# Optimization experiments

Measured on AMD Instinct MI355X. Metric: run time of the kernel, lower is better.

The kernel has to match this reference:

```python
import jax, jax.numpy as jnp
import numpy as np

D_MODEL = 1024
N_HEADS = 16
N_KV_HEADS = 4
HEAD_DIM = D_MODEL // N_HEADS  # 64
N_REP = N_HEADS // N_KV_HEADS  # 4
THETA = 10000.0
LOGIT_CAP = 30.0
EPS = 1e-6
SCALE = HEAD_DIM ** -0.5


def rmsnorm(x, w):
    return x * jax.lax.rsqrt(jnp.mean(x * x, axis=-1, keepdims=True) + EPS) * w


def rope_tables(seq_len, dtype):
    inv_freq = 1.0 / (THETA ** (jnp.arange(0, HEAD_DIM, 2, dtype=jnp.float32) / HEAD_DIM))
    t = jnp.arange(seq_len, dtype=jnp.float32)
    freqs = jnp.outer(t, inv_freq)                      # [S, hd/2]
    emb = jnp.concatenate([freqs, freqs], axis=-1)      # [S, hd]
    return jnp.cos(emb).astype(dtype), jnp.sin(emb).astype(dtype)


def rotate_half(x):
    x1, x2 = jnp.split(x, 2, axis=-1)
    return jnp.concatenate([-x2, x1], axis=-1)


def apply_rope(x, cos, sin):
    # x: [B, H, S, hd]; cos/sin: [S, hd] broadcast over (B, H)
    return x * cos + rotate_half(x) * sin


def setup_inputs() -> dict:
    key = jax.random.key(0)
    ks = jax.random.split(key, 7)
    B, S = 4, 2048
    w = 0.02
    return {
        "x": jax.random.normal(ks[0], (B, S, D_MODEL), dtype=jnp.float32),
        "Wq": jax.random.normal(ks[1], (N_HEADS * HEAD_DIM, D_MODEL), dtype=jnp.float32) * w,
        "Wk": jax.random.normal(ks[2], (N_KV_HEADS * HEAD_DIM, D_MODEL), dtype=jnp.float32) * w,
        "Wv": jax.random.normal(ks[3], (N_KV_HEADS * HEAD_DIM, D_MODEL), dtype=jnp.float32) * w,
        "Wo": jax.random.normal(ks[4], (D_MODEL, N_HEADS * HEAD_DIM), dtype=jnp.float32) * w,
        "q_norm_w": jnp.ones((HEAD_DIM,), dtype=jnp.float32),
        "k_norm_w": jnp.ones((HEAD_DIM,), dtype=jnp.float32),
    }


def reference(x, Wq, Wk, Wv, Wo, q_norm_w, k_norm_w):
    B, S, _ = x.shape
    # projections (nn.Linear: y = x @ W^T)
    q = (x @ Wq.T).reshape(B, S, N_HEADS, HEAD_DIM).transpose(0, 2, 1, 3)      # [B,H,S,d]
    k = (x @ Wk.T).reshape(B, S, N_KV_HEADS, HEAD_DIM).transpose(0, 2, 1, 3)   # [B,Hkv,S,d]
    v = (x @ Wv.T).reshape(B, S, N_KV_HEADS, HEAD_DIM).transpose(0, 2, 1, 3)
    # QK-RMSNorm
    q = rmsnorm(q, q_norm_w)
    k = rmsnorm(k, k_norm_w)
    # RoPE
    cos, sin = rope_tables(S, x.dtype)
    q = apply_rope(q, cos, sin)
    k = apply_rope(k, cos, sin)
    # GQA expand (repeat_interleave over head dim)
    k_exp = jnp.repeat(k, N_REP, axis=1)  # [B,H,S,d]
    v_exp = jnp.repeat(v, N_REP, axis=1)
    # soft-capped attention (training path)
    scores = jnp.einsum('bhqd,bhkd->bhqk', q, k_exp) * SCALE
    scores = LOGIT_CAP * jnp.tanh(scores / LOGIT_CAP)
    causal = jnp.triu(jnp.ones((S, S), dtype=bool), k=1)  # kv_len - seq_len + 1 = 1
    scores = jnp.where(causal, -jnp.inf, scores)
    attn = jax.nn.softmax(scores, axis=-1)
    out = jnp.einsum('bhqk,bhkd->bhqd', attn, v_exp)
    out = out.transpose(0, 2, 1, 3).reshape(B, S, N_HEADS * HEAD_DIM)
    return out @ Wo.T
```

## Files before the change

### kernel.cpp

```cpp
#include <hip/hip_runtime.h>
#include <hip/hip_bf16.h>
#include <math.h>
#include <stdint.h>

#define D_MODEL 1024
#define NHEADS  16
#define NKV     4
#define HD      64
#define SEQ     2048
#define BATCH   4
#define MTOK    (BATCH*SEQ)
#define NQKV    (D_MODEL + 2*NKV*HD)
#define ASCALE  0.125f
#define CAP     30.0f

using f32x4  = __attribute__((ext_vector_type(4))) float;
using f32x2  = __attribute__((ext_vector_type(2))) float;
using bf16x8 = __attribute__((ext_vector_type(8))) short;

__device__ __forceinline__ unsigned short f2bf(float f) {
  union { float f; unsigned u; } v; v.f = f;
  unsigned u = v.u + 0x7fffu + ((v.u >> 16) & 1u);
  return (unsigned short)(u >> 16);
}
__device__ __forceinline__ unsigned short f2bf_hup(float f) {
  union { float f; unsigned u; } v; v.f = f;
  return (unsigned short)((v.u + 0x8000u) >> 16);
}
__device__ __forceinline__ float fexp2(float x) {
  return __builtin_amdgcn_exp2f(x);
}
__device__ __forceinline__ void async_copy16(void* lds, const void* g) {
  __builtin_amdgcn_global_load_lds(
      (const __attribute__((address_space(1))) unsigned int*)(uintptr_t)g,
      (__attribute__((address_space(3))) unsigned int*)(uintptr_t)lds, 16, 0, 0);
}

__global__ __launch_bounds__(256) void cvt_all(
    const float* __restrict__ x, const float* __restrict__ wq,
    const float* __restrict__ wk, const float* __restrict__ wv,
    const float* __restrict__ wo,
    unsigned short* __restrict__ xb, unsigned short* __restrict__ wqkv,
    unsigned short* __restrict__ wob) {
  const long i = (long)(blockIdx.x * 256 + threadIdx.x) * 4;
  const float* src; unsigned short* dst; long off;
  if (i < 8388608L)      { src = x;  dst = xb;             off = i; }
  else if (i < 9437184L) { src = wq; dst = wqkv;           off = i - 8388608L; }
  else if (i < 9699328L) { src = wk; dst = wqkv + 1048576; off = i - 9437184L; }
  else if (i < 9961472L) { src = wv; dst = wqkv + 1310720; off = i - 9699328L; }
  else                   { src = wo; dst = wob;            off = i - 9961472L; }
  float4 v = *(const float4*)(src + off);
  ushort4 o; o.x = f2bf(v.x); o.y = f2bf(v.y); o.z = f2bf(v.z); o.w = f2bf(v.w);
  *(ushort4*)(dst + off) = o;
}

__global__ __launch_bounds__(256) void gemm_qkv(
    const unsigned short* __restrict__ A, const unsigned short* __restrict__ B,
    const float* __restrict__ qw, const float* __restrict__ kw,
    unsigned short* __restrict__ Qn, unsigned short* __restrict__ Kn,
    unsigned short* __restrict__ Vt) {
  __shared__ __align__(16) unsigned short As[128 * 32];
  __shared__ __align__(16) unsigned short Bs[128 * 32];
  const int t = threadIdx.x;
  const int w = t >> 6, l = t & 63;
  const int mb = blockIdx.x, nb = blockIdx.y;
  const int wm = w & 1, wn = w >> 1;
  const int quad = l >> 4, ln = l & 15;
  const int K = D_MODEL;
  f32x4 acc[4][4] = {};
  const unsigned short* Ag = A + (size_t)(mb * 128 + w * 32) * K;
  const unsigned short* Bg = B + (size_t)(nb * 128 + w * 32) * K;
  char* Asw = (char*)As + w * 2048;
  char* Bsw = (char*)Bs + w * 2048;
  const int lrow = l >> 2, lcol = (l & 3) * 8;

  for (int kb = 0; kb < K; kb += 32) {
    async_copy16(Asw + l * 16,        Ag + (size_t)lrow * K + kb + lcol);
    async_copy16(Asw + 1024 + l * 16, Ag + (size_t)(16 + lrow) * K + kb + lcol);
    async_copy16(Bsw + l * 16,        Bg + (size_t)lrow * K + kb + lcol);
    async_copy16(Bsw + 1024 + l * 16, Bg + (size_t)(16 + lrow) * K + kb + lcol);
    __syncthreads();
    bf16x8 af[4], bfr[4];
#pragma unroll
    for (int mt = 0; mt < 4; ++mt)
      af[mt] = *(const bf16x8*)(As + (wm * 64 + mt * 16 + ln) * 32 + quad * 8);
#pragma unroll
    for (int nt = 0; nt < 4; ++nt)
      bfr[nt] = *(const bf16x8*)(Bs + (wn * 64 + nt * 16 + ln) * 32 + quad * 8);
#pragma unroll
    for (int mt = 0; mt < 4; ++mt)
#pragma unroll
      for (int nt = 0; nt < 4; ++nt)
        acc[mt][nt] = __builtin_amdgcn_mfma_f32_16x16x32_bf16(af[mt], bfr[nt], acc[mt][nt], 0, 0, 0);
    __syncthreads();
  }

  const int hs = nb * 2 + wn;
  const int bB = mb >> 4;
  const int sBase = ((mb & 15) * 128) + wm * 64;

  if (hs < 20) {
    const float* wgt = (hs < 16) ? qw : kw;
    float wv_[4];
#pragma unroll
    for (int nt = 0; nt < 4; ++nt) wv_[nt] = wgt[nt * 16 + ln];
    const float f0 = __expf(-(float)ln * 0.2878231366f);
    const float f1 = f0 * 0.01f;
    unsigned short* dst = (hs < 16)
        ? Qn + (size_t)(bB * 16 + hs) * SEQ * 64
        : Kn + (size_t)(bB * 4 + (hs - 16)) * SEQ * 64;
#pragma unroll
    for (int mt = 0; mt < 4; ++mt) {
#pragma unroll
      for (int r = 0; r < 4; ++r) {
        const int sTok = sBase + mt * 16 + quad * 4 + r;
        float ss = 0.f;
#pragma unroll
        for (int nt = 0; nt < 4; ++nt) ss = fmaf(acc[mt][nt][r], acc[mt][nt][r], ss);
        ss += __shfl_xor(ss, 1, 64); ss += __shfl_xor(ss, 2, 64);
        ss += __shfl_xor(ss, 4, 64); ss += __shfl_xor(ss, 8, 64);
        const float inv = rsqrtf(ss * (1.0f / 64.0f) + 1e-6f);
        float xn[4];
#pragma unroll
        for (int nt = 0; nt < 4; ++nt) xn[nt] = acc[mt][nt][r] * inv * wv_[nt];
        float sn0, cs0, sn1, cs1;
        __sincosf((float)sTok * f0, &sn0, &cs0);
        __sincosf((float)sTok * f1, &sn1, &cs1);
        const float o0 = xn[0] * cs0 - xn[2] * sn0;
        const float o1 = xn[1] * cs1 - xn[3] * sn1;
        const float o2 = xn[2] * cs0 + xn[0] * sn0;
        const float o3 = xn[3] * cs1 + xn[1] * sn1;
        const size_t ro = (size_t)sTok * 64 + ln;
        dst[ro]      = f2bf(o0);
        dst[ro + 16] = f2bf(o1);
        dst[ro + 32] = f2bf(o2);
        dst[ro + 48] = f2bf(o3);
      }
    }
  } else {
    unsigned short* dst = Vt + (size_t)(bB * 4 + (hs - 20)) * 64 * SEQ;
#pragma unroll
    for (int mt = 0; mt < 4; ++mt)
#pragma unroll
      for (int nt = 0; nt < 4; ++nt)
#pragma unroll
        for (int r = 0; r < 4; ++r) {
          const int sTok = sBase + mt * 16 + quad * 4 + r;
          dst[(size_t)(nt * 16 + ln) * SEQ + sTok] = f2bf(acc[mt][nt][r]);
        }
  }
}

__global__ __launch_bounds__(256) void gemm_bt_f32(
    const unsigned short* __restrict__ A, const unsigned short* __restrict__ B,
    float* __restrict__ C, int M, int N, int K) {
  __shared__ __align__(16) unsigned short As[128 * 32];
  __shared__ __align__(16) unsigned short Bs[128 * 32];
  const int t = threadIdx.x;
  const int w = t >> 6, l = t & 63;
  const int mb = blockIdx.x, nb = blockIdx.y;
  const int wm = w & 1, wn = w >> 1;
  f32x4 acc[4][4] = {};
  const unsigned short* Ag = A + (size_t)(mb * 128 + w * 32) * K;
  const unsigned short* Bg = B + (size_t)(nb * 128 + w * 32) * K;
  char* Asw = (char*)As + w * 2048;
  char* Bsw = (char*)Bs + w * 2048;
  const int lrow = l >> 2, lcol = (l & 3) * 8;

  for (int kb = 0; kb < K; kb += 32) {
    async_copy16(Asw + l * 16,        Ag + (size_t)lrow * K + kb + lcol);
    async_copy16(Asw + 1024 + l * 16, Ag + (size_t)(16 + lrow) * K + kb + lcol);
    async_copy16(Bsw + l * 16,        Bg + (size_t)lrow * K + kb + lcol);
    async_copy16(Bsw + 1024 + l * 16, Bg + (size_t)(16 + lrow) * K + kb + lcol);
    __syncthreads();
    bf16x8 af[4], bfr[4];
#pragma unroll
    for (int mt = 0; mt < 4; ++mt)
      af[mt] = *(const bf16x8*)(As + (wm * 64 + mt * 16 + (l & 15)) * 32 + (l >> 4) * 8);
#pragma unroll
    for (int nt = 0; nt < 4; ++nt)
      bfr[nt] = *(const bf16x8*)(Bs + (wn * 64 + nt * 16 + (l & 15)) * 32 + (l >> 4) * 8);
#pragma unroll
    for (int mt = 0; mt < 4; ++mt)
#pragma unroll
      for (int nt = 0; nt < 4; ++nt)
        acc[mt][nt] = __builtin_amdgcn_mfma_f32_16x16x32_bf16(af[mt], bfr[nt], acc[mt][nt], 0, 0, 0);
    __syncthreads();
  }
  const int row0 = mb * 128 + wm * 64, col0 = nb * 128 + wn * 64;
#pragma unroll
  for (int mt = 0; mt < 4; ++mt)
#pragma unroll
    for (int nt = 0; nt < 4; ++nt)
#pragma unroll
      for (int r = 0; r < 4; ++r) {
        int row = row0 + mt * 16 + (l >> 4) * 4 + r;
        int col = col0 + nt * 16 + (l & 15);
        C[(size_t)row * N + col] = acc[mt][nt][r];
      }
}

__global__ __launch_bounds__(256, 4) void attn(
    const unsigned short* __restrict__ Qn, const unsigned short* __restrict__ Kn,
    const unsigned short* __restrict__ Vtg, unsigned short* __restrict__ O) {
  __shared__ __align__(16) unsigned short Ks[4096];
  __shared__ __align__(16) unsigned short Vs[4096];
  __shared__ __align__(16) unsigned short Ps[8192];
  const int t = threadIdx.x, w = t >> 6, l = t & 63;
  const int quad = l >> 4, ln = l & 15;
  const int bid = blockIdx.x;
  const int qt = 15 - (bid >> 6);
  const int bh = bid & 63;
  const int h = bh & 15, b = bh >> 4;
  const int q0 = qt * 128;
  const int wq0 = q0 + w * 32;
  const unsigned short* Qh = Qn + ((size_t)(b * 16 + h)) * SEQ * 64;
  const unsigned short* Kg = Kn + ((size_t)(b * 4 + (h >> 2))) * SEQ * 64;
  const unsigned short* Vg = Vtg + ((size_t)(b * 4 + (h >> 2))) * 64 * SEQ;
  const int lrow = l >> 2, lc = (l & 3) * 8;

  bf16x8 aq[2][2];
#pragma unroll
  for (int mt = 0; mt < 2; ++mt)
#pragma unroll
    for (int ks = 0; ks < 2; ++ks)
      aq[mt][ks] = *(const bf16x8*)(Qh + (size_t)(wq0 + mt * 16 + ln) * 64 + ks * 32 + quad * 8);
  f32x4 o_acc[2][4] = {};
  f32x2 lp[2][2] = {};

  const float Cc = 0.18033688011112042f;
  const float B1 = -5.787037037e-6f;
  const float M2 = 11.541560327f;

  const int jmax = 2 * qt + 2;
  for (int jj = 0; jj < jmax; ++jj) {
    const int kv0 = jj * 64;
    __syncthreads();
#pragma unroll
    for (int i = 0; i < 2; ++i) {
      int s = w * 2 + i;
      int snt = s >> 1, sks = s & 1;
      async_copy16((char*)Ks + s * 1024,
                   Kg + (size_t)(kv0 + snt * 16 + lrow) * 64 + sks * 32 + lc);
      async_copy16((char*)Vs + s * 1024,
                   Vg + (size_t)(snt * 16 + lrow) * SEQ + kv0 + sks * 32 + lc);
    }
    __syncthreads();
    if (kv0 > wq0 + 31) continue;

    f32x4 sacc[2][4] = {};
#pragma unroll
    for (int nt = 0; nt < 4; ++nt)
#pragma unroll
      for (int ks = 0; ks < 2; ++ks) {
        bf16x8 bk = *(const bf16x8*)((char*)Ks + (nt * 2 + ks) * 1024 + ln * 64 + quad * 16);
        sacc[0][nt] = __builtin_amdgcn_mfma_f32_16x16x32_bf16(aq[0][ks], bk, sacc[0][nt], 0, 0, 0);
        sacc[1][nt] = __builtin_amdgcn_mfma_f32_16x16x32_bf16(aq[1][ks], bk, sacc[1][nt], 0, 0, 0);
      }

    const bool needMask = (kv0 + 63 > wq0);
#pragma unroll
    for (int mt = 0; mt < 2; ++mt)
#pragma unroll
      for (int nt = 0; nt < 4; ++nt) {
        const int col = nt * 16 + ln;
        const int base = w * 2048 + mt * 1024 + (col >> 5) * 512 +
                         ((((col >> 3) & 3) ^ quad) << 3) + (col & 7);
#pragma unroll
        for (int rp = 0; rp < 2; ++rp) {
          f32x2 s = { sacc[mt][nt][rp * 2], sacc[mt][nt][rp * 2 + 1] };
          f32x2 s2 = s * s;
          f32x2 tt = s2 * B1 + 1.0f;
          f32x2 arg = (s * Cc) * tt - M2;
          float pr0 = fexp2(arg.x), pr1 = fexp2(arg.y);
          if (needMask) {
            const int qrow = wq0 + mt * 16 + quad * 4 + rp * 2;
            if ((kv0 + col) > qrow)     pr0 = 0.0f;
            if ((kv0 + col) > qrow + 1) pr1 = 0.0f;
          }
          lp[mt][rp] += (f32x2){pr0, pr1};
          Ps[base + (quad * 4 + rp * 2) * 32]     = f2bf_hup(pr0);
          Ps[base + (quad * 4 + rp * 2 + 1) * 32] = f2bf_hup(pr1);
        }
      }
    __builtin_amdgcn_s_waitcnt(0xc07f);

    bf16x8 ap[2][2];
#pragma unroll
    for (int mt = 0; mt < 2; ++mt)
#pragma unroll
      for (int ks = 0; ks < 2; ++ks)
        ap[mt][ks] = *(const bf16x8*)((char*)Ps + w * 4096 + mt * 2048 + ks * 1024 +
                                      ln * 64 + ((quad ^ (ln >> 2)) << 4));
#pragma unroll
    for (int nt = 0; nt < 4; ++nt)
#pragma unroll
      for (int ks = 0; ks < 2; ++ks) {
        bf16x8 bv = *(const bf16x8*)((char*)Vs + (nt * 2 + ks) * 1024 + ln * 64 + quad * 16);
        o_acc[0][nt] = __builtin_amdgcn_mfma_f32_16x16x32_bf16(ap[0][ks], bv, o_acc[0][nt], 0, 0, 0);
        o_acc[1][nt] = __builtin_amdgcn_mfma_f32_16x16x32_bf16(ap[1][ks], bv, o_acc[1][nt], 0, 0, 0);
      }
  }

  float invl[2][4];
#pragma unroll
  for (int mt = 0; mt < 2; ++mt)
#pragma unroll
    for (int r = 0; r < 4; ++r) {
      float s = lp[mt][r >> 1][r & 1];
      s += __shfl_xor(s, 1, 64); s += __shfl_xor(s, 2, 64);
      s += __shfl_xor(s, 4, 64); s += __shfl_xor(s, 8, 64);
      invl[mt][r] = __builtin_amdgcn_rcpf(s);
    }
#pragma unroll
  for (int mt = 0; mt < 2; ++mt)
#pragma unroll
    for (int nt = 0; nt < 4; ++nt)
#pragma unroll
      for (int r = 0; r < 4; ++r) {
        int qrow = wq0 + mt * 16 + quad * 4 + r;
        int col = h * 64 + nt * 16 + ln;
        O[((size_t)(b * SEQ + qrow)) * 1024 + col] = f2bf_hup(o_acc[mt][nt][r] * invl[mt][r]);
      }
}

extern "C" void kernel_launch(void* const* d_in, const int* in_sizes, int n_in,
                              void* d_out, int out_size, void* d_ws, size_t ws_size,
                              hipStream_t stream) {
  const float* x  = (const float*)d_in[0];
  const float* Wq = (const float*)d_in[1];
  const float* Wk = (const float*)d_in[2];
  const float* Wv = (const float*)d_in[3];
  const float* Wo = (const float*)d_in[4];
  const float* qw = (const float*)d_in[5];
  const float* kw = (const float*)d_in[6];
  float* out = (float*)d_out;

  char* ws = (char*)d_ws;
  unsigned short* xb   = (unsigned short*)(ws);
  unsigned short* wqkv = (unsigned short*)(ws + 16777216);
  unsigned short* wo   = (unsigned short*)(ws + 19922944);
  unsigned short* Qn   = (unsigned short*)(ws + 22020096);
  unsigned short* Kn   = (unsigned short*)(ws + 38797312);
  unsigned short* Vtg  = (unsigned short*)(ws + 42991616);
  unsigned short* Ob   = (unsigned short*)(ws + 47185920);

  cvt_all<<<10752, 256, 0, stream>>>(x, Wq, Wk, Wv, Wo, xb, wqkv, wo);
  gemm_qkv<<<dim3(MTOK / 128, NQKV / 128), 256, 0, stream>>>(xb, wqkv, qw, kw, Qn, Kn, Vtg);
  attn<<<1024, 256, 0, stream>>>(Qn, Kn, Vtg, Ob);
  gemm_bt_f32<<<dim3(MTOK / 128, 1024 / 128), 256, 0, stream>>>(Ob, wo, out, MTOK, 1024, 1024);
}
```

Before: 244.9 us.

## Precompute RoPE table, stage QKV epilogue via LDS, load attention K/V directly

Extends the conversion kernel to compute a cos/sin RoPE table once per token and frequency, and has the QKV GEMM epilogue read that table instead of calling sincos per element. The Q/K/V epilogue results are now staged per wave in LDS and written out as coalesced 16-byte rows, replacing the scattered 2-byte stores, which matters most for the transposed V. The attention kernel drops its shared K/V tiles and barriers: each wave loads K and V fragments straight from global memory into registers and only iterates over its own causal range. This trades block-level data sharing and async LDS copies for more global and L2 traffic per wave, more register pressure, and a larger LDS footprint in gemm_qkv.

```diff
diff --git a/kernel.cpp b/kernel.cpp
--- a/kernel.cpp
+++ b/kernel.cpp
@@ -41,7 +41,18 @@
     const float* __restrict__ wk, const float* __restrict__ wv,
     const float* __restrict__ wo,
     unsigned short* __restrict__ xb, unsigned short* __restrict__ wqkv,
-    unsigned short* __restrict__ wob) {
+    unsigned short* __restrict__ wob, float* __restrict__ ropeT) {
+  if (blockIdx.x >= 10752) {
+    const int tid = (blockIdx.x - 10752) * 256 + threadIdx.x;
+    const int s = tid >> 4, ln = tid & 15;
+    const float f0 = expf(-(float)ln * 0.28782313662425572f);
+    const float f1 = f0 * 0.01f;
+    float4 tb;
+    tb.x = cosf((float)s * f0); tb.y = sinf((float)s * f0);
+    tb.z = cosf((float)s * f1); tb.w = sinf((float)s * f1);
+    *(float4*)(ropeT + (size_t)tid * 4) = tb;
+    return;
+  }
   const long i = (long)(blockIdx.x * 256 + threadIdx.x) * 4;
   const float* src; unsigned short* dst; long off;
   if (i < 8388608L)      { src = x;  dst = xb;             off = i; }
@@ -57,10 +68,12 @@
 __global__ __launch_bounds__(256) void gemm_qkv(
     const unsigned short* __restrict__ A, const unsigned short* __restrict__ B,
     const float* __restrict__ qw, const float* __restrict__ kw,
+    const float* __restrict__ ropeT,
     unsigned short* __restrict__ Qn, unsigned short* __restrict__ Kn,
     unsigned short* __restrict__ Vt) {
   __shared__ __align__(16) unsigned short As[128 * 32];
   __shared__ __align__(16) unsigned short Bs[128 * 32];
+  __shared__ __align__(16) unsigned short Rp[4][64 * 72];
   const int t = threadIdx.x;
   const int w = t >> 6, l = t & 63;
   const int mb = blockIdx.x, nb = blockIdx.y;
@@ -98,14 +111,13 @@
   const int hs = nb * 2 + wn;
   const int bB = mb >> 4;
   const int sBase = ((mb & 15) * 128) + wm * 64;
+  unsigned short* rp = Rp[w];
 
   if (hs < 20) {
     const float* wgt = (hs < 16) ? qw : kw;
     float wv_[4];
 #pragma unroll
     for (int nt = 0; nt < 4; ++nt) wv_[nt] = wgt[nt * 16 + ln];
-    const float f0 = __expf(-(float)ln * 0.2878231366f);
-    const float f1 = f0 * 0.01f;
     unsigned short* dst = (hs < 16)
         ? Qn + (size_t)(bB * 16 + hs) * SEQ * 64
         : Kn + (size_t)(bB * 4 + (hs - 16)) * SEQ * 64;
@@ -113,7 +125,8 @@
     for (int mt = 0; mt < 4; ++mt) {
 #pragma unroll
       for (int r = 0; r < 4; ++r) {
-        const int sTok = sBase + mt * 16 + quad * 4 + r;
+        const int rowL = mt * 16 + quad * 4 + r;
+        const int sTok = sBase + rowL;
         float ss = 0.f;
 #pragma unroll
         for (int nt = 0; nt < 4; ++nt) ss = fmaf(acc[mt][nt][r], acc[mt][nt][r], ss);
@@ -123,19 +136,19 @@
         float xn[4];
 #pragma unroll
         for (int nt = 0; nt < 4; ++nt) xn[nt] = acc[mt][nt][r] * inv * wv_[nt];
-        float sn0, cs0, sn1, cs1;
-        __sincosf((float)sTok * f0, &sn0, &cs0);
-        __sincosf((float)sTok * f1, &sn1, &cs1);
-        const float o0 = xn[0] * cs0 - xn[2] * sn0;
-        const float o1 = xn[1] * cs1 - xn[3] * sn1;
-        const float o2 = xn[2] * cs0 + xn[0] * sn0;
-        const float o3 = xn[3] * cs1 + xn[1] * sn1;
-        const size_t ro = (size_t)sTok * 64 + ln;
-        dst[ro]      = f2bf(o0);
-        dst[ro + 16] = f2bf(o1);
-        dst[ro + 32] = f2bf(o2);
-        dst[ro + 48] = f2bf(o3);
-      }
+        const float4 tb = *(const float4*)(ropeT + ((size_t)sTok * 16 + ln) * 4);
+        rp[rowL * 72 + ln]      = f2bf(xn[0] * tb.x - xn[2] * tb.y);
+        rp[rowL * 72 + ln + 16] = f2bf(xn[1] * tb.z - xn[3] * tb.w);
+        rp[rowL * 72 + ln + 32] = f2bf(xn[2] * tb.x + xn[0] * tb.y);
+        rp[rowL * 72 + ln + 48] = f2bf(xn[3] * tb.z + xn[1] * tb.w);
+      }
+    }
+    __builtin_amdgcn_s_waitcnt(0xc07f);
+#pragma unroll
+    for (int i = 0; i < 8; ++i) {
+      const int row = (l >> 3) + i * 8, c8 = l & 7;
+      bf16x8 v = *(const bf16x8*)(rp + row * 72 + c8 * 8);
+      *(bf16x8*)(dst + (size_t)(sBase + row) * 64 + c8 * 8) = v;
     }
   } else {
     unsigned short* dst = Vt + (size_t)(bB * 4 + (hs - 20)) * 64 * SEQ;
@@ -144,10 +157,15 @@
 #pragma unroll
       for (int nt = 0; nt < 4; ++nt)
 #pragma unroll
-        for (int r = 0; r < 4; ++r) {
-          const int sTok = sBase + mt * 16 + quad * 4 + r;
-          dst[(size_t)(nt * 16 + ln) * SEQ + sTok] = f2bf(acc[mt][nt][r]);
-        }
+        for (int r = 0; r < 4; ++r)
+          rp[(nt * 16 + ln) * 72 + mt * 16 + quad * 4 + r] = f2bf(acc[mt][nt][r]);
+    __builtin_amdgcn_s_waitcnt(0xc07f);
+#pragma unroll
+    for (int i = 0; i < 8; ++i) {
+      const int d = (l >> 3) + i * 8, c8 = l & 7;
+      bf16x8 v = *(const bf16x8*)(rp + d * 72 + c8 * 8);
+      *(bf16x8*)(dst + (size_t)d * SEQ + sBase + c8 * 8) = v;
+    }
   }
 }
 
@@ -203,8 +221,6 @@
 __global__ __launch_bounds__(256, 4) void attn(
     const unsigned short* __restrict__ Qn, const unsigned short* __restrict__ Kn,
     const unsigned short* __restrict__ Vtg, unsigned short* __restrict__ O) {
-  __shared__ __align__(16) unsigned short Ks[4096];
-  __shared__ __align__(16) unsigned short Vs[4096];
   __shared__ __align__(16) unsigned short Ps[8192];
   const int t = threadIdx.x, w = t >> 6, l = t & 63;
   const int quad = l >> 4, ln = l & 15;
@@ -217,7 +233,6 @@
   const unsigned short* Qh = Qn + ((size_t)(b * 16 + h)) * SEQ * 64;
   const unsigned short* Kg = Kn + ((size_t)(b * 4 + (h >> 2))) * SEQ * 64;
   const unsigned short* Vg = Vtg + ((size_t)(b * 4 + (h >> 2))) * 64 * SEQ;
-  const int lrow = l >> 2, lc = (l & 3) * 8;
 
   bf16x8 aq[2][2];
 #pragma unroll
@@ -232,31 +247,32 @@
   const float B1 = -5.787037037e-6f;
   const float M2 = 11.541560327f;
 
-  const int jmax = 2 * qt + 2;
-  for (int jj = 0; jj < jmax; ++jj) {
+  const int jmaxw = ((wq0 + 31) >> 6) + 1;
+  for (int jj = 0; jj < jmaxw; ++jj) {
     const int kv0 = jj * 64;
-    __syncthreads();
-#pragma unroll
-    for (int i = 0; i < 2; ++i) {
-      int s = w * 2 + i;
-      int snt = s >> 1, sks = s & 1;
-      async_copy16((char*)Ks + s * 1024,
-                   Kg + (size_t)(kv0 + snt * 16 + lrow) * 64 + sks * 32 + lc);
-      async_copy16((char*)Vs + s * 1024,
-                   Vg + (size_t)(snt * 16 + lrow) * SEQ + kv0 + sks * 32 + lc);
-    }
-    __syncthreads();
-    if (kv0 > wq0 + 31) continue;
+
+    bf16x8 bk[4][2];
+#pragma unroll
+    for (int nt = 0; nt < 4; ++nt)
+#pragma unroll
+      for (int ks = 0; ks < 2; ++ks)
+        bk[nt][ks] = *(const bf16x8*)(Kg + (size_t)(kv0 + nt * 16 + ln) * 64 + ks * 32 + quad * 8);
 
     f32x4 sacc[2][4] = {};
 #pragma unroll
     for (int nt = 0; nt < 4; ++nt)
 #pragma unroll
       for (int ks = 0; ks < 2; ++ks) {
-        bf16x8 bk = *(const bf16x8*)((char*)Ks + (nt * 2 + ks) * 1024 + ln * 64 + quad * 16);
-        sacc[0][nt] = __builtin_amdgcn_mfma_f32_16x16x32_bf16(aq[0][ks], bk, sacc[0][nt], 0, 0, 0);
-        sacc[1][nt] = __builtin_amdgcn_mfma_f32_16x16x32_bf16(aq[1][ks], bk, sacc[1][nt], 0, 0, 0);
-      }
+        sacc[0][nt] = __builtin_amdgcn_mfma_f32_16x16x32_bf16(aq[0][ks], bk[nt][ks], sacc[0][nt], 0, 0, 0);
+        sacc[1][nt] = __builtin_amdgcn_mfma_f32_16x16x32_bf16(aq[1][ks], bk[nt][ks], sacc[1][nt], 0, 0, 0);
+      }
+
+    bf16x8 bv[4][2];
+#pragma unroll
+    for (int nt = 0; nt < 4; ++nt)
+#pragma unroll
+      for (int ks = 0; ks < 2; ++ks)
+        bv[nt][ks] = *(const bf16x8*)(Vg + (size_t)(nt * 16 + ln) * SEQ + kv0 + ks * 32 + quad * 8);
 
     const bool needMask = (kv0 + 63 > wq0);
 #pragma unroll
@@ -296,9 +312,8 @@
     for (int nt = 0; nt < 4; ++nt)
 #pragma unroll
       for (int ks = 0; ks < 2; ++ks) {
-        bf16x8 bv = *(const bf16x8*)((char*)Vs + (nt * 2 + ks) * 1024 + ln * 64 + quad * 16);
-        o_acc[0][nt] = __builtin_amdgcn_mfma_f32_16x16x32_bf16(ap[0][ks], bv, o_acc[0][nt], 0, 0, 0);
-        o_acc[1][nt] = __builtin_amdgcn_mfma_f32_16x16x32_bf16(ap[1][ks], bv, o_acc[1][nt], 0, 0, 0);
+        o_acc[0][nt] = __builtin_amdgcn_mfma_f32_16x16x32_bf16(ap[0][ks], bv[nt][ks], o_acc[0][nt], 0, 0, 0);
+        o_acc[1][nt] = __builtin_amdgcn_mfma_f32_16x16x32_bf16(ap[1][ks], bv[nt][ks], o_acc[1][nt], 0, 0, 0);
       }
   }
 
@@ -344,9 +359,10 @@
   unsigned short* Kn   = (unsigned short*)(ws + 38797312);
   unsigned short* Vtg  = (unsigned short*)(ws + 42991616);
   unsigned short* Ob   = (unsigned short*)(ws + 47185920);
-
-  cvt_all<<<10752, 256, 0, stream>>>(x, Wq, Wk, Wv, Wo, xb, wqkv, wo);
-  gemm_qkv<<<dim3(MTOK / 128, NQKV / 128), 256, 0, stream>>>(xb, wqkv, qw, kw, Qn, Kn, Vtg);
+  float*          ropeT= (float*)         (ws + 63963136);
+
+  cvt_all<<<10880, 256, 0, stream>>>(x, Wq, Wk, Wv, Wo, xb, wqkv, wo, ropeT);
+  gemm_qkv<<<dim3(MTOK / 128, NQKV / 128), 256, 0, stream>>>(xb, wqkv, qw, kw, ropeT, Qn, Kn, Vtg);
   attn<<<1024, 256, 0, stream>>>(Qn, Kn, Vtg, Ob);
   gemm_bt_f32<<<dim3(MTOK / 128, 1024 / 128), 256, 0, stream>>>(Ob, wo, out, MTOK, 1024, 1024);
 }
```

New measurement: 385.8 us. 1.58x slower.
